# Kernel tuning notes

Hardware: AMD Instinct MI355X
Metric: run time of the kernel (lower is better)

The kernel has to match this reference:

```python
import jax, jax.numpy as jnp
import numpy as np

EPS = 1e-8

def _unit(v):
    # matches unitization(): v / (||v|| + 1e-8), norm over last (xyz) axis
    return v / (jnp.linalg.norm(v, axis=-1, keepdims=True) + EPS)

def setup_inputs() -> dict:
    key = jax.random.key(0)
    ks = jax.random.split(key, 6)
    B, C, P, S = 16, 76, 1024, 32  # 12 + C_in(=64) channels
    inp = jax.random.normal(ks[0], (B, C, P, S), jnp.float32)
    normal = jax.random.normal(ks[1], (B, P, 3), jnp.float32)
    w1 = jax.random.normal(ks[2], (128, 73), jnp.float32) * 0.1
    b1 = jnp.zeros((128,), jnp.float32)
    w2 = jax.random.normal(ks[3], (128, 128), jnp.float32) * 0.1
    b2 = jnp.zeros((128,), jnp.float32)
    return {"input": inp, "normal": normal, "w1": w1, "b1": b1, "w2": w2, "b2": b2}

def reference(input, normal, w1, b1, w2, b2):
    # channel layout: [0:3]=abs coords, [3:6]=neighbor normals, [6:9]=relative coords,
    # [9:12]=neighbor azimuth dirs, [12:]=input features (C_in=64)
    other_normal = input[:, 3:6]   # (B,3,P,S)
    rel = input[:, 6:9]            # (B,3,P,S)
    other_dir = input[:, 9:12]     # (B,3,P,S)
    feats = input[:, 12:]          # (B,C_in,P,S)

    # azimuth vector: mean of relative coords over neighbors excluding centroid slot
    azi = jnp.mean(rel[:, :, :, 1:], axis=3).transpose(0, 2, 1)  # (B,P,3)

    # PointAlign rotation: local frame with z = unit normal,
    # x = azimuth projected onto tangent plane, y = z x x (row-stacked rotation)
    n = _unit(normal)
    a = _unit(azi)
    xax = _unit(a - jnp.sum(a * n, axis=-1, keepdims=True) * n)
    yax = jnp.cross(n, xax)
    R = jnp.stack([xax, yax, n], axis=2)  # (B,P,3,3)

    def align(v):  # (B,3,P,S) -> (B,3,P,S): rotate each neighbor vector into local frame
        return jnp.einsum('bpij,bjps->bips', R, v)

    azi_u = _unit(azi)                                  # (B,P,3)
    dir_dif = align(azi_u.transpose(0, 2, 1)[:, :, :, None] - other_dir)

    # x[:,0:3] = aligned relative coords, then concat other_normal + dir_difs
    x = jnp.concatenate([align(rel), feats, align(other_normal), dir_dif], axis=1)  # (B,73,P,S)

    # shared MLP: two 1x1 convs + ReLU
    h = jax.nn.relu(jnp.einsum('oc,bcps->bops', w1, x) + b1[None, :, None, None])
    h = jax.nn.relu(jnp.einsum('oc,bcps->bops', w2, h) + b2[None, :, None, None])

    pooled = jnp.max(h, axis=3)  # max_pool2d over nsample -> (B,128,P)
    # not last layer: prepend unit azimuth vector
    return jnp.concatenate([azi_u.transpose(0, 2, 1), pooled], axis=1)  # (B,131,P)
```

## Files before the change

kernel.cpp:

```cpp
#include <hip/hip_runtime.h>
#include <hip/hip_bf16.h>

#define NB 16
#define NP 1024
#define NS 32
#define NC 76
#define XSTR 104
#define HSTR 136
#define TPB 16

typedef __attribute__((ext_vector_type(8))) short bf16x8;
typedef __attribute__((ext_vector_type(4))) float f32x4;

__device__ inline short f2bf(float f) {
  unsigned u = __builtin_bit_cast(unsigned, f);
  u = u + 0x7fffu + ((u >> 16) & 1u);
  return (short)(u >> 16);
}
__device__ inline unsigned cvt_pk_bf16(float lo, float hi) {
  unsigned r;
  asm("v_cvt_pk_bf16_f32 %0, %1, %2" : "=v"(r) : "v"(lo), "v"(hi));
  return r;
}
__device__ inline int swzx(int col, int k) {
  return (col * XSTR + k) ^ (((col >> 4) & 7) << 3);
}
__device__ inline int swzh(int col, int k) {
  return (col * HSTR + k) ^ (((col >> 4) & 7) << 3);
}
__device__ inline float dpp_max16(float v) {
  int x;
  x = __builtin_amdgcn_update_dpp(0, __builtin_bit_cast(int, v), 0xB1, 0xf, 0xf, true);
  v = fmaxf(v, __builtin_bit_cast(float, x));
  x = __builtin_amdgcn_update_dpp(0, __builtin_bit_cast(int, v), 0x4E, 0xf, 0xf, true);
  v = fmaxf(v, __builtin_bit_cast(float, x));
  x = __builtin_amdgcn_update_dpp(0, __builtin_bit_cast(int, v), 0x141, 0xf, 0xf, true);
  v = fmaxf(v, __builtin_bit_cast(float, x));
  x = __builtin_amdgcn_update_dpp(0, __builtin_bit_cast(int, v), 0x140, 0xf, 0xf, true);
  v = fmaxf(v, __builtin_bit_cast(float, x));
  return v;
}

__global__ void frames_kernel(const float* __restrict__ inp,
                              const float* __restrict__ normal,
                              float* __restrict__ out, float* __restrict__ ws) {
  const int bp = blockIdx.x * 256 + threadIdx.x;
  const int b = bp >> 10, p = bp & 1023;

  float azi[3];
#pragma unroll
  for (int i = 0; i < 3; ++i) {
    const float* row = inp + (size_t)((b*NC + 6 + i)*NP + p) * NS;
    float s = 0.f;
#pragma unroll
    for (int q = 0; q < 8; ++q) {
      float4 v = ((const float4*)row)[q];
      s += (v.x + v.y) + (v.z + v.w);
    }
    s -= row[0];
    azi[i] = s / 31.f;
  }
  float nr[3];
#pragma unroll
  for (int i = 0; i < 3; ++i) nr[i] = normal[(size_t)(b*NP + p)*3 + i];
  float nn = sqrtf(nr[0]*nr[0] + nr[1]*nr[1] + nr[2]*nr[2]) + 1e-8f;
  nr[0] /= nn; nr[1] /= nn; nr[2] /= nn;
  float au[3] = {azi[0], azi[1], azi[2]};
  float an = sqrtf(au[0]*au[0] + au[1]*au[1] + au[2]*au[2]) + 1e-8f;
  au[0] /= an; au[1] /= an; au[2] /= an;
  float d = au[0]*nr[0] + au[1]*nr[1] + au[2]*nr[2];
  float xax[3] = {au[0] - d*nr[0], au[1] - d*nr[1], au[2] - d*nr[2]};
  float xn = sqrtf(xax[0]*xax[0] + xax[1]*xax[1] + xax[2]*xax[2]) + 1e-8f;
  xax[0] /= xn; xax[1] /= xn; xax[2] /= xn;
  float yax[3] = {nr[1]*xax[2] - nr[2]*xax[1],
                  nr[2]*xax[0] - nr[0]*xax[2],
                  nr[0]*xax[1] - nr[1]*xax[0]};
#pragma unroll
  for (int i = 0; i < 3; ++i)
    out[(size_t)(b*131 + i)*NP + p] = au[i];

  float* w = ws + (size_t)bp * 12;
  w[0]=xax[0]; w[1]=xax[1]; w[2]=xax[2];
  w[3]=yax[0]; w[4]=yax[1]; w[5]=yax[2];
  w[6]=nr[0];  w[7]=nr[1];  w[8]=nr[2];
  w[9]  = xax[0]*au[0] + xax[1]*au[1] + xax[2]*au[2];
  w[10] = yax[0]*au[0] + yax[1]*au[1] + yax[2]*au[2];
  w[11] = nr[0]*au[0]  + nr[1]*au[1]  + nr[2]*au[2];
}

__global__ __launch_bounds__(512, 2)
void mlp_kernel(const float* __restrict__ inp, const float* __restrict__ w1g,
                const float* __restrict__ b1g, const float* __restrict__ w2g,
                const float* __restrict__ b2g, const float* __restrict__ ws,
                float* __restrict__ out) {
  __shared__ short xb[128 * XSTR];
  __shared__ short hb[128 * HSTR];
  const int tid = threadIdx.x;
  const int lane = tid & 63;
  const int wv = tid >> 6;
  const int wr = wv >> 1;
  const int wc = wv & 1;
  const int l15 = lane & 15;
  const int l4 = lane >> 4;

  const int tile0 = blockIdx.x * TPB;

  const int s4  = tid & 7;
  const int flp = (tid >> 3) & 3;
  const int chq = tid >> 5;
  const int colb = flp*32 + 4*s4;

  bf16x8 w1f[2][3];
#pragma unroll
  for (int mf = 0; mf < 2; ++mf)
#pragma unroll
    for (int ks = 0; ks < 3; ++ks) {
      bf16x8 a;
#pragma unroll
      for (int j = 0; j < 8; ++j) {
        int row = 32*wr + 16*mf + l15;
        int kk = 32*ks + 8*l4 + j;
        float v = 0.f;
        if (kk < 73) {
          int c = (kk < 64) ? (kk + 3) : ((kk < 67) ? (kk - 64) : kk);
          v = w1g[row*73 + c];
        } else if (kk == 73) {
          v = b1g[row];
        }
        a[j] = f2bf(v);
      }
      w1f[mf][ks] = a;
    }
  bf16x8 w2f[2][4];
#pragma unroll
  for (int mf = 0; mf < 2; ++mf)
#pragma unroll
    for (int ks = 0; ks < 4; ++ks) {
      bf16x8 a;
#pragma unroll
      for (int j = 0; j < 8; ++j) {
        int row = 32*wr + 16*mf + l15;
        int kk = 32*ks + 8*l4 + j;
        a[j] = f2bf(w2g[row*128 + kk]);
      }
      w2f[mf][ks] = a;
    }
  float bias2[2][4];
#pragma unroll
  for (int mf = 0; mf < 2; ++mf)
#pragma unroll
    for (int r = 0; r < 4; ++r)
      bias2[mf][r] = b2g[32*wr + 16*mf + 4*l4 + r];

  for (int i = tid; i < 128*23; i += 512) {
    int col = i / 23;
    int k = 73 + (i - col*23);
    xb[swzx(col, k)] = (k == 73) ? (short)0x3F80 : (short)0;
  }

  float4 sf0, sf1, sf2, sf3;
  auto stage = [&](int it2) {
    const int tile = tile0 + it2;
    const int bb = tile >> 8;
    const int pb = (tile & 255) * 4;
    const float* base = inp + ((size_t)((bb*NC + 12 + 4*chq)*NP) + pb + flp)*NS + 4*s4;
    sf0 = *(const float4*)(base + 0*(size_t)NP*NS);
    sf1 = *(const float4*)(base + 1*(size_t)NP*NS);
    sf2 = *(const float4*)(base + 2*(size_t)NP*NS);
    sf3 = *(const float4*)(base + 3*(size_t)NP*NS);
  };
  auto fill = [&](int it2) {
    const float* f0 = (const float*)&sf0;
    const float* f1 = (const float*)&sf1;
    const float* f2 = (const float*)&sf2;
    const float* f3 = (const float*)&sf3;
#pragma unroll
    for (int j = 0; j < 4; ++j) {
      uint2 pk;
      pk.x = cvt_pk_bf16(f0[j], f1[j]);
      pk.y = cvt_pk_bf16(f2[j], f3[j]);
      *(uint2*)&xb[swzx(colb + j, 4*chq)] = pk;
    }
    if (tid < 128) {
      const int tile = tile0 + it2;
      const int bb = tile >> 8;
      const int pb = (tile & 255) * 4;
      const int col = tid;
      const int lp = col >> 5, s = col & 31;
      const int p = pb + lp;
      const float* Rp = ws + (size_t)(bb*NP + p)*12;
      float R[12];
#pragma unroll
      for (int i = 0; i < 12; ++i) R[i] = Rp[i];
      float rel[3], on[3], od[3];
#pragma unroll
      for (int i = 0; i < 3; ++i) {
        rel[i] = inp[(size_t)((bb*NC + 6 + i)*NP + p)*NS + s];
        on[i]  = inp[(size_t)((bb*NC + 3 + i)*NP + p)*NS + s];
        od[i]  = inp[(size_t)((bb*NC + 9 + i)*NP + p)*NS + s];
      }
      float xv[9];
#pragma unroll
      for (int r = 0; r < 3; ++r) {
        xv[r]   = R[3*r]*rel[0] + R[3*r+1]*rel[1] + R[3*r+2]*rel[2];
        xv[3+r] = R[3*r]*on[0]  + R[3*r+1]*on[1]  + R[3*r+2]*on[2];
        xv[6+r] = R[9+r] - (R[3*r]*od[0] + R[3*r+1]*od[1] + R[3*r+2]*od[2]);
      }
      int4 pk;
      pk.x = (int)cvt_pk_bf16(xv[0], xv[1]);
      pk.y = (int)cvt_pk_bf16(xv[2], xv[3]);
      pk.z = (int)cvt_pk_bf16(xv[4], xv[5]);
      pk.w = (int)cvt_pk_bf16(xv[6], xv[7]);
      *(int4*)&xb[swzx(col, 64)] = pk;
      xb[swzx(col, 72)] = f2bf(xv[8]);
    }
  };

  stage(0);
  fill(0);
  stage(1);
  __syncthreads();

  for (int it = 0; it < TPB; ++it) {
    const int tile = tile0 + it;
    const int bb = tile >> 8;
    const int pb = (tile & 255) * 4;

    f32x4 acc1[2][4];
#pragma unroll
    for (int mf = 0; mf < 2; ++mf)
#pragma unroll
      for (int nf = 0; nf < 4; ++nf) acc1[mf][nf] = f32x4{0.f,0.f,0.f,0.f};
#pragma unroll
    for (int ks = 0; ks < 3; ++ks) {
      bf16x8 bv[4];
#pragma unroll
      for (int nf = 0; nf < 4; ++nf)
        bv[nf] = *(const bf16x8*)&xb[swzx(64*wc + 16*nf + l15, 32*ks + 8*l4)];
#pragma unroll
      for (int mf = 0; mf < 2; ++mf)
#pragma unroll
        for (int nf = 0; nf < 4; ++nf)
          acc1[mf][nf] = __builtin_amdgcn_mfma_f32_16x16x32_bf16(
              w1f[mf][ks], bv[nf], acc1[mf][nf], 0, 0, 0);
    }

#pragma unroll
    for (int mf = 0; mf < 2; ++mf)
#pragma unroll
      for (int nf = 0; nf < 4; ++nf) {
        const int col = 64*wc + 16*nf + l15;
        const int row0 = 32*wr + 16*mf + 4*l4;
        uint2 pk;
        pk.x = cvt_pk_bf16(fmaxf(acc1[mf][nf][0], 0.f), fmaxf(acc1[mf][nf][1], 0.f));
        pk.y = cvt_pk_bf16(fmaxf(acc1[mf][nf][2], 0.f), fmaxf(acc1[mf][nf][3], 0.f));
        *(uint2*)&hb[swzh(col, row0)] = pk;
      }
    __syncthreads();

    if (it + 1 < TPB) fill(it + 1);
    if (it + 2 < TPB) stage(it + 2);

    f32x4 acc2[2][4];
#pragma unroll
    for (int mf = 0; mf < 2; ++mf)
#pragma unroll
      for (int nf = 0; nf < 4; ++nf) acc2[mf][nf] = f32x4{0.f,0.f,0.f,0.f};
#pragma unroll
    for (int ks = 0; ks < 4; ++ks) {
      bf16x8 bv[4];
#pragma unroll
      for (int nf = 0; nf < 4; ++nf)
        bv[nf] = *(const bf16x8*)&hb[swzh(64*wc + 16*nf + l15, 32*ks + 8*l4)];
#pragma unroll
      for (int mf = 0; mf < 2; ++mf)
#pragma unroll
        for (int nf = 0; nf < 4; ++nf)
          acc2[mf][nf] = __builtin_amdgcn_mfma_f32_16x16x32_bf16(
              w2f[mf][ks], bv[nf], acc2[mf][nf], 0, 0, 0);
    }

#pragma unroll
    for (int mf = 0; mf < 2; ++mf)
#pragma unroll
      for (int r = 0; r < 4; ++r) {
        float v0 = fmaxf(acc2[mf][0][r], acc2[mf][1][r]);
        float v1 = fmaxf(acc2[mf][2][r], acc2[mf][3][r]);
        v0 = dpp_max16(v0);
        v1 = dpp_max16(v1);
        v0 = fmaxf(v0 + bias2[mf][r], 0.f);
        v1 = fmaxf(v1 + bias2[mf][r], 0.f);
        if (l15 == 0) {
          const int row = 32*wr + 16*mf + 4*l4 + r;
          *(float2*)&out[(size_t)(bb*131 + 3 + row)*NP + pb + 2*wc] = float2{v0, v1};
        }
      }
    __syncthreads();
  }
}

extern "C" void kernel_launch(void* const* d_in, const int* in_sizes, int n_in,
                              void* d_out, int out_size, void* d_ws, size_t ws_size,
                              hipStream_t stream) {
  const float* inp    = (const float*)d_in[0];
  const float* normal = (const float*)d_in[1];
  const float* w1     = (const float*)d_in[2];
  const float* b1     = (const float*)d_in[3];
  const float* w2     = (const float*)d_in[4];
  const float* b2     = (const float*)d_in[5];
  float* out = (float*)d_out;
  float* ws  = (float*)d_ws;

  frames_kernel<<<dim3((NB*NP)/256), dim3(256), 0, stream>>>(inp, normal, out, ws);
  mlp_kernel<<<dim3(NB*NP/4/TPB), dim3(512), 0, stream>>>(inp, w1, b1, w2, b2, ws, out);
}
```

Before: 63.06 us.

## Fuse frame computation into MLP kernel and double-buffer LDS across tiles

```diff
diff --git a/kernel.cpp b/kernel.cpp
--- a/kernel.cpp
+++ b/kernel.cpp
@@ -41,60 +41,13 @@
   return v;
 }
 
-__global__ void frames_kernel(const float* __restrict__ inp,
-                              const float* __restrict__ normal,
-                              float* __restrict__ out, float* __restrict__ ws) {
-  const int bp = blockIdx.x * 256 + threadIdx.x;
-  const int b = bp >> 10, p = bp & 1023;
-
-  float azi[3];
-#pragma unroll
-  for (int i = 0; i < 3; ++i) {
-    const float* row = inp + (size_t)((b*NC + 6 + i)*NP + p) * NS;
-    float s = 0.f;
-#pragma unroll
-    for (int q = 0; q < 8; ++q) {
-      float4 v = ((const float4*)row)[q];
-      s += (v.x + v.y) + (v.z + v.w);
-    }
-    s -= row[0];
-    azi[i] = s / 31.f;
-  }
-  float nr[3];
-#pragma unroll
-  for (int i = 0; i < 3; ++i) nr[i] = normal[(size_t)(b*NP + p)*3 + i];
-  float nn = sqrtf(nr[0]*nr[0] + nr[1]*nr[1] + nr[2]*nr[2]) + 1e-8f;
-  nr[0] /= nn; nr[1] /= nn; nr[2] /= nn;
-  float au[3] = {azi[0], azi[1], azi[2]};
-  float an = sqrtf(au[0]*au[0] + au[1]*au[1] + au[2]*au[2]) + 1e-8f;
-  au[0] /= an; au[1] /= an; au[2] /= an;
-  float d = au[0]*nr[0] + au[1]*nr[1] + au[2]*nr[2];
-  float xax[3] = {au[0] - d*nr[0], au[1] - d*nr[1], au[2] - d*nr[2]};
-  float xn = sqrtf(xax[0]*xax[0] + xax[1]*xax[1] + xax[2]*xax[2]) + 1e-8f;
-  xax[0] /= xn; xax[1] /= xn; xax[2] /= xn;
-  float yax[3] = {nr[1]*xax[2] - nr[2]*xax[1],
-                  nr[2]*xax[0] - nr[0]*xax[2],
-                  nr[0]*xax[1] - nr[1]*xax[0]};
-#pragma unroll
-  for (int i = 0; i < 3; ++i)
-    out[(size_t)(b*131 + i)*NP + p] = au[i];
-
-  float* w = ws + (size_t)bp * 12;
-  w[0]=xax[0]; w[1]=xax[1]; w[2]=xax[2];
-  w[3]=yax[0]; w[4]=yax[1]; w[5]=yax[2];
-  w[6]=nr[0];  w[7]=nr[1];  w[8]=nr[2];
-  w[9]  = xax[0]*au[0] + xax[1]*au[1] + xax[2]*au[2];
-  w[10] = yax[0]*au[0] + yax[1]*au[1] + yax[2]*au[2];
-  w[11] = nr[0]*au[0]  + nr[1]*au[1]  + nr[2]*au[2];
-}
-
 __global__ __launch_bounds__(512, 2)
 void mlp_kernel(const float* __restrict__ inp, const float* __restrict__ w1g,
                 const float* __restrict__ b1g, const float* __restrict__ w2g,
-                const float* __restrict__ b2g, const float* __restrict__ ws,
+                const float* __restrict__ b2g, const float* __restrict__ normal,
                 float* __restrict__ out) {
-  __shared__ short xb[128 * XSTR];
-  __shared__ short hb[128 * HSTR];
+  __shared__ short xb[2][128 * XSTR];
+  __shared__ short hb[2][128 * HSTR];
   const int tid = threadIdx.x;
   const int lane = tid & 63;
   const int wv = tid >> 6;
@@ -152,13 +105,16 @@
     for (int r = 0; r < 4; ++r)
       bias2[mf][r] = b2g[32*wr + 16*mf + 4*l4 + r];
 
-  for (int i = tid; i < 128*23; i += 512) {
-    int col = i / 23;
-    int k = 73 + (i - col*23);
-    xb[swzx(col, k)] = (k == 73) ? (short)0x3F80 : (short)0;
+  for (int i = tid; i < 2*128*23; i += 512) {
+    int bufi = i / (128*23);
+    int r = i - bufi*(128*23);
+    int col = r / 23;
+    int k = 73 + (r - col*23);
+    xb[bufi][swzx(col, k)] = (k == 73) ? (short)0x3F80 : (short)0;
   }
 
   float4 sf0, sf1, sf2, sf3;
+  float sro[9];
   auto stage = [&](int it2) {
     const int tile = tile0 + it2;
     const int bb = tile >> 8;
@@ -168,8 +124,19 @@
     sf1 = *(const float4*)(base + 1*(size_t)NP*NS);
     sf2 = *(const float4*)(base + 2*(size_t)NP*NS);
     sf3 = *(const float4*)(base + 3*(size_t)NP*NS);
+    if (tid < 128) {
+      const int lp = tid >> 5, s = tid & 31;
+      const int p = pb + lp;
+#pragma unroll
+      for (int i = 0; i < 3; ++i) {
+        sro[i]   = inp[(size_t)((bb*NC + 6 + i)*NP + p)*NS + s];
+        sro[3+i] = inp[(size_t)((bb*NC + 3 + i)*NP + p)*NS + s];
+        sro[6+i] = inp[(size_t)((bb*NC + 9 + i)*NP + p)*NS + s];
+      }
+    }
   };
-  auto fill = [&](int it2) {
+
+  auto fill = [&](int it2, int bufi) {
     const float* f0 = (const float*)&sf0;
     const float* f1 = (const float*)&sf1;
     const float* f2 = (const float*)&sf2;
@@ -179,7 +146,7 @@
       uint2 pk;
       pk.x = cvt_pk_bf16(f0[j], f1[j]);
       pk.y = cvt_pk_bf16(f2[j], f3[j]);
-      *(uint2*)&xb[swzx(colb + j, 4*chq)] = pk;
+      *(uint2*)&xb[bufi][swzx(colb + j, 4*chq)] = pk;
     }
     if (tid < 128) {
       const int tile = tile0 + it2;
@@ -188,55 +155,66 @@
       const int col = tid;
       const int lp = col >> 5, s = col & 31;
       const int p = pb + lp;
-      const float* Rp = ws + (size_t)(bb*NP + p)*12;
-      float R[12];
-#pragma unroll
-      for (int i = 0; i < 12; ++i) R[i] = Rp[i];
-      float rel[3], on[3], od[3];
+      float az[3];
 #pragma unroll
       for (int i = 0; i < 3; ++i) {
-        rel[i] = inp[(size_t)((bb*NC + 6 + i)*NP + p)*NS + s];
-        on[i]  = inp[(size_t)((bb*NC + 3 + i)*NP + p)*NS + s];
-        od[i]  = inp[(size_t)((bb*NC + 9 + i)*NP + p)*NS + s];
+        float sum = sro[i];
+#pragma unroll
+        for (int m = 1; m < 32; m <<= 1) sum += __shfl_xor(sum, m);
+        float v0 = __shfl(sro[i], lane & 32);
+        az[i] = (sum - v0) * (1.f/31.f);
+      }
+      float nr[3];
+#pragma unroll
+      for (int i = 0; i < 3; ++i) nr[i] = normal[(size_t)(bb*NP + p)*3 + i];
+      float nn = sqrtf(nr[0]*nr[0] + nr[1]*nr[1] + nr[2]*nr[2]) + 1e-8f;
+      nr[0] /= nn; nr[1] /= nn; nr[2] /= nn;
+      float an = sqrtf(az[0]*az[0] + az[1]*az[1] + az[2]*az[2]) + 1e-8f;
+      float au[3] = {az[0]/an, az[1]/an, az[2]/an};
+      float d = au[0]*nr[0] + au[1]*nr[1] + au[2]*nr[2];
+      float xax[3] = {au[0] - d*nr[0], au[1] - d*nr[1], au[2] - d*nr[2]};
+      float xn = sqrtf(xax[0]*xax[0] + xax[1]*xax[1] + xax[2]*xax[2]) + 1e-8f;
+      xax[0] /= xn; xax[1] /= xn; xax[2] /= xn;
+      float yax[3] = {nr[1]*xax[2] - nr[2]*xax[1],
+                      nr[2]*xax[0] - nr[0]*xax[2],
+                      nr[0]*xax[1] - nr[1]*xax[0]};
+      if (s < 3) {
+        float o = (s == 0) ? au[0] : ((s == 1) ? au[1] : au[2]);
+        out[(size_t)(bb*131 + s)*NP + p] = o;
       }
       float xv[9];
 #pragma unroll
       for (int r = 0; r < 3; ++r) {
-        xv[r]   = R[3*r]*rel[0] + R[3*r+1]*rel[1] + R[3*r+2]*rel[2];
-        xv[3+r] = R[3*r]*on[0]  + R[3*r+1]*on[1]  + R[3*r+2]*on[2];
-        xv[6+r] = R[9+r] - (R[3*r]*od[0] + R[3*r+1]*od[1] + R[3*r+2]*od[2]);
+        const float* Rr = (r == 0) ? xax : ((r == 1) ? yax : nr);
+        xv[r]   = Rr[0]*sro[0] + Rr[1]*sro[1] + Rr[2]*sro[2];
+        xv[3+r] = Rr[0]*sro[3] + Rr[1]*sro[4] + Rr[2]*sro[5];
+        xv[6+r] = (Rr[0]*au[0] + Rr[1]*au[1] + Rr[2]*au[2])
+                - (Rr[0]*sro[6] + Rr[1]*sro[7] + Rr[2]*sro[8]);
       }
       int4 pk;
       pk.x = (int)cvt_pk_bf16(xv[0], xv[1]);
       pk.y = (int)cvt_pk_bf16(xv[2], xv[3]);
       pk.z = (int)cvt_pk_bf16(xv[4], xv[5]);
       pk.w = (int)cvt_pk_bf16(xv[6], xv[7]);
-      *(int4*)&xb[swzx(col, 64)] = pk;
-      xb[swzx(col, 72)] = f2bf(xv[8]);
+      *(int4*)&xb[bufi][swzx(col, 64)] = pk;
+      xb[bufi][swzx(col, 72)] = f2bf(xv[8]);
     }
   };
 
-  stage(0);
-  fill(0);
-  stage(1);
-  __syncthreads();
-
-  for (int it = 0; it < TPB; ++it) {
-    const int tile = tile0 + it;
-    const int bb = tile >> 8;
-    const int pb = (tile & 255) * 4;
-
+  f32x4 acc2[2][4];
+  auto layer1_h1 = [&](int tt) {
     f32x4 acc1[2][4];
 #pragma unroll
     for (int mf = 0; mf < 2; ++mf)
 #pragma unroll
       for (int nf = 0; nf < 4; ++nf) acc1[mf][nf] = f32x4{0.f,0.f,0.f,0.f};
+    const short* xs = xb[tt & 1];
 #pragma unroll
     for (int ks = 0; ks < 3; ++ks) {
       bf16x8 bv[4];
 #pragma unroll
       for (int nf = 0; nf < 4; ++nf)
-        bv[nf] = *(const bf16x8*)&xb[swzx(64*wc + 16*nf + l15, 32*ks + 8*l4)];
+        bv[nf] = *(const bf16x8*)&xs[swzx(64*wc + 16*nf + l15, 32*ks + 8*l4)];
 #pragma unroll
       for (int mf = 0; mf < 2; ++mf)
 #pragma unroll
@@ -244,7 +222,7 @@
           acc1[mf][nf] = __builtin_amdgcn_mfma_f32_16x16x32_bf16(
               w1f[mf][ks], bv[nf], acc1[mf][nf], 0, 0, 0);
     }
-
+    short* hs = hb[tt & 1];
 #pragma unroll
     for (int mf = 0; mf < 2; ++mf)
 #pragma unroll
@@ -254,24 +232,21 @@
         uint2 pk;
         pk.x = cvt_pk_bf16(fmaxf(acc1[mf][nf][0], 0.f), fmaxf(acc1[mf][nf][1], 0.f));
         pk.y = cvt_pk_bf16(fmaxf(acc1[mf][nf][2], 0.f), fmaxf(acc1[mf][nf][3], 0.f));
-        *(uint2*)&hb[swzh(col, row0)] = pk;
-      }
-    __syncthreads();
-
-    if (it + 1 < TPB) fill(it + 1);
-    if (it + 2 < TPB) stage(it + 2);
-
-    f32x4 acc2[2][4];
+        *(uint2*)&hs[swzh(col, row0)] = pk;
+      }
+  };
+  auto layer2 = [&](int tt) {
 #pragma unroll
     for (int mf = 0; mf < 2; ++mf)
 #pragma unroll
       for (int nf = 0; nf < 4; ++nf) acc2[mf][nf] = f32x4{0.f,0.f,0.f,0.f};
+    const short* hs = hb[tt & 1];
 #pragma unroll
     for (int ks = 0; ks < 4; ++ks) {
       bf16x8 bv[4];
 #pragma unroll
       for (int nf = 0; nf < 4; ++nf)
-        bv[nf] = *(const bf16x8*)&hb[swzh(64*wc + 16*nf + l15, 32*ks + 8*l4)];
+        bv[nf] = *(const bf16x8*)&hs[swzh(64*wc + 16*nf + l15, 32*ks + 8*l4)];
 #pragma unroll
       for (int mf = 0; mf < 2; ++mf)
 #pragma unroll
@@ -279,6 +254,23 @@
           acc2[mf][nf] = __builtin_amdgcn_mfma_f32_16x16x32_bf16(
               w2f[mf][ks], bv[nf], acc2[mf][nf], 0, 0, 0);
     }
+  };
+
+  stage(0);
+  fill(0, 0);
+  stage(1);
+  __syncthreads();
+  layer1_h1(0);
+  fill(1, 1);
+  stage(2);
+  __syncthreads();
+
+  for (int it = 0; it < TPB; ++it) {
+    const int tile = tile0 + it;
+    const int bb = tile >> 8;
+    const int pb = (tile & 255) * 4;
+
+    layer2(it);
 
 #pragma unroll
     for (int mf = 0; mf < 2; ++mf)
@@ -295,7 +287,11 @@
           *(float2*)&out[(size_t)(bb*131 + 3 + row)*NP + pb + 2*wc] = float2{v0, v1};
         }
       }
-    __syncthreads();
+
+    if (it + 1 < TPB) layer1_h1(it + 1);
+    if (it + 2 < TPB) fill(it + 2, it & 1);
+    if (it + 3 < TPB) stage(it + 3);
+    if (it + 1 < TPB) __syncthreads();
   }
 }
 
@@ -309,8 +305,7 @@
   const float* w2     = (const float*)d_in[4];
   const float* b2     = (const float*)d_in[5];
   float* out = (float*)d_out;
-  float* ws  = (float*)d_ws;
-
-  frames_kernel<<<dim3((NB*NP)/256), dim3(256), 0, stream>>>(inp, normal, out, ws);
-  mlp_kernel<<<dim3(NB*NP/4/TPB), dim3(512), 0, stream>>>(inp, w1, b1, w2, b2, ws, out);
-}
+
+  mlp_kernel<<<dim3(NB*NP/4/TPB), dim3(512), 0, stream>>>(
+      inp, w1, b1, w2, b2, normal, out);
+}
```

Result: faster. 60.82 us (-3.6%).

## Fuse frame computation into MLP kernel via wavefront shuffles, halve tiles per block

Applied to the files above, without the earlier changes.

```diff
diff --git a/kernel.cpp b/kernel.cpp
--- a/kernel.cpp
+++ b/kernel.cpp
@@ -7,7 +7,7 @@
 #define NC 76
 #define XSTR 104
 #define HSTR 136
-#define TPB 16
+#define TPB 8
 
 typedef __attribute__((ext_vector_type(8))) short bf16x8;
 typedef __attribute__((ext_vector_type(4))) float f32x4;
@@ -41,57 +41,10 @@
   return v;
 }
 
-__global__ void frames_kernel(const float* __restrict__ inp,
-                              const float* __restrict__ normal,
-                              float* __restrict__ out, float* __restrict__ ws) {
-  const int bp = blockIdx.x * 256 + threadIdx.x;
-  const int b = bp >> 10, p = bp & 1023;
-
-  float azi[3];
-#pragma unroll
-  for (int i = 0; i < 3; ++i) {
-    const float* row = inp + (size_t)((b*NC + 6 + i)*NP + p) * NS;
-    float s = 0.f;
-#pragma unroll
-    for (int q = 0; q < 8; ++q) {
-      float4 v = ((const float4*)row)[q];
-      s += (v.x + v.y) + (v.z + v.w);
-    }
-    s -= row[0];
-    azi[i] = s / 31.f;
-  }
-  float nr[3];
-#pragma unroll
-  for (int i = 0; i < 3; ++i) nr[i] = normal[(size_t)(b*NP + p)*3 + i];
-  float nn = sqrtf(nr[0]*nr[0] + nr[1]*nr[1] + nr[2]*nr[2]) + 1e-8f;
-  nr[0] /= nn; nr[1] /= nn; nr[2] /= nn;
-  float au[3] = {azi[0], azi[1], azi[2]};
-  float an = sqrtf(au[0]*au[0] + au[1]*au[1] + au[2]*au[2]) + 1e-8f;
-  au[0] /= an; au[1] /= an; au[2] /= an;
-  float d = au[0]*nr[0] + au[1]*nr[1] + au[2]*nr[2];
-  float xax[3] = {au[0] - d*nr[0], au[1] - d*nr[1], au[2] - d*nr[2]};
-  float xn = sqrtf(xax[0]*xax[0] + xax[1]*xax[1] + xax[2]*xax[2]) + 1e-8f;
-  xax[0] /= xn; xax[1] /= xn; xax[2] /= xn;
-  float yax[3] = {nr[1]*xax[2] - nr[2]*xax[1],
-                  nr[2]*xax[0] - nr[0]*xax[2],
-                  nr[0]*xax[1] - nr[1]*xax[0]};
-#pragma unroll
-  for (int i = 0; i < 3; ++i)
-    out[(size_t)(b*131 + i)*NP + p] = au[i];
-
-  float* w = ws + (size_t)bp * 12;
-  w[0]=xax[0]; w[1]=xax[1]; w[2]=xax[2];
-  w[3]=yax[0]; w[4]=yax[1]; w[5]=yax[2];
-  w[6]=nr[0];  w[7]=nr[1];  w[8]=nr[2];
-  w[9]  = xax[0]*au[0] + xax[1]*au[1] + xax[2]*au[2];
-  w[10] = yax[0]*au[0] + yax[1]*au[1] + yax[2]*au[2];
-  w[11] = nr[0]*au[0]  + nr[1]*au[1]  + nr[2]*au[2];
-}
-
-__global__ __launch_bounds__(512, 2)
+__global__ __launch_bounds__(512, 4)
 void mlp_kernel(const float* __restrict__ inp, const float* __restrict__ w1g,
                 const float* __restrict__ b1g, const float* __restrict__ w2g,
-                const float* __restrict__ b2g, const float* __restrict__ ws,
+                const float* __restrict__ b2g, const float* __restrict__ normal,
                 float* __restrict__ out) {
   __shared__ short xb[128 * XSTR];
   __shared__ short hb[128 * HSTR];
@@ -169,6 +122,7 @@
     sf2 = *(const float4*)(base + 2*(size_t)NP*NS);
     sf3 = *(const float4*)(base + 3*(size_t)NP*NS);
   };
+
   auto fill = [&](int it2) {
     const float* f0 = (const float*)&sf0;
     const float* f1 = (const float*)&sf1;
@@ -188,10 +142,6 @@
       const int col = tid;
       const int lp = col >> 5, s = col & 31;
       const int p = pb + lp;
-      const float* Rp = ws + (size_t)(bb*NP + p)*12;
-      float R[12];
-#pragma unroll
-      for (int i = 0; i < 12; ++i) R[i] = Rp[i];
       float rel[3], on[3], od[3];
 #pragma unroll
       for (int i = 0; i < 3; ++i) {
@@ -199,12 +149,41 @@
         on[i]  = inp[(size_t)((bb*NC + 3 + i)*NP + p)*NS + s];
         od[i]  = inp[(size_t)((bb*NC + 9 + i)*NP + p)*NS + s];
       }
+      float az[3];
+#pragma unroll
+      for (int i = 0; i < 3; ++i) {
+        float sum = rel[i];
+#pragma unroll
+        for (int m = 1; m < 32; m <<= 1) sum += __shfl_xor(sum, m);
+        float v0 = __shfl(rel[i], lane & 32);
+        az[i] = (sum - v0) * (1.f/31.f);
+      }
+      float nr[3];
+#pragma unroll
+      for (int i = 0; i < 3; ++i) nr[i] = normal[(size_t)(bb*NP + p)*3 + i];
+      float nn = sqrtf(nr[0]*nr[0] + nr[1]*nr[1] + nr[2]*nr[2]) + 1e-8f;
+      nr[0] /= nn; nr[1] /= nn; nr[2] /= nn;
+      float an = sqrtf(az[0]*az[0] + az[1]*az[1] + az[2]*az[2]) + 1e-8f;
+      float au[3] = {az[0]/an, az[1]/an, az[2]/an};
+      float d = au[0]*nr[0] + au[1]*nr[1] + au[2]*nr[2];
+      float xax[3] = {au[0] - d*nr[0], au[1] - d*nr[1], au[2] - d*nr[2]};
+      float xn = sqrtf(xax[0]*xax[0] + xax[1]*xax[1] + xax[2]*xax[2]) + 1e-8f;
+      xax[0] /= xn; xax[1] /= xn; xax[2] /= xn;
+      float yax[3] = {nr[1]*xax[2] - nr[2]*xax[1],
+                      nr[2]*xax[0] - nr[0]*xax[2],
+                      nr[0]*xax[1] - nr[1]*xax[0]};
+      if (s < 3) {
+        float o = (s == 0) ? au[0] : ((s == 1) ? au[1] : au[2]);
+        out[(size_t)(bb*131 + s)*NP + p] = o;
+      }
       float xv[9];
 #pragma unroll
       for (int r = 0; r < 3; ++r) {
-        xv[r]   = R[3*r]*rel[0] + R[3*r+1]*rel[1] + R[3*r+2]*rel[2];
-        xv[3+r] = R[3*r]*on[0]  + R[3*r+1]*on[1]  + R[3*r+2]*on[2];
-        xv[6+r] = R[9+r] - (R[3*r]*od[0] + R[3*r+1]*od[1] + R[3*r+2]*od[2]);
+        const float* Rr = (r == 0) ? xax : ((r == 1) ? yax : nr);
+        xv[r]   = Rr[0]*rel[0] + Rr[1]*rel[1] + Rr[2]*rel[2];
+        xv[3+r] = Rr[0]*on[0]  + Rr[1]*on[1]  + Rr[2]*on[2];
+        xv[6+r] = (Rr[0]*au[0] + Rr[1]*au[1] + Rr[2]*au[2])
+                - (Rr[0]*od[0] + Rr[1]*od[1] + Rr[2]*od[2]);
       }
       int4 pk;
       pk.x = (int)cvt_pk_bf16(xv[0], xv[1]);
@@ -244,7 +223,6 @@
           acc1[mf][nf] = __builtin_amdgcn_mfma_f32_16x16x32_bf16(
               w1f[mf][ks], bv[nf], acc1[mf][nf], 0, 0, 0);
     }
-
 #pragma unroll
     for (int mf = 0; mf < 2; ++mf)
 #pragma unroll
@@ -309,8 +287,7 @@
   const float* w2     = (const float*)d_in[4];
   const float* b2     = (const float*)d_in[5];
   float* out = (float*)d_out;
-  float* ws  = (float*)d_ws;
-
-  frames_kernel<<<dim3((NB*NP)/256), dim3(256), 0, stream>>>(inp, normal, out, ws);
-  mlp_kernel<<<dim3(NB*NP/4/TPB), dim3(512), 0, stream>>>(inp, w1, b1, w2, b2, ws, out);
-}
+
+  mlp_kernel<<<dim3(NB*NP/4/TPB), dim3(512), 0, stream>>>(
+      inp, w1, b1, w2, b2, normal, out);
+}
```

After: 237.9 us. 277% more time.
